# Kernel optimization log

Measured on AMD Instinct MI355X. Metric: run time of the kernel, lower is better.

## Reference

```python
import jax, jax.numpy as jnp
import numpy as np

N_NODES = 50000
N_EDGES = 800000
IN_CH = 128
OUT_CH = 64
H1, C1 = 8, 8            # conv1: heads=8, out=8, concat -> 64
H2, C2 = 1, OUT_CH       # conv2: heads=1, out=64, concat=False
NEG_SLOPE = 0.2


def gat_conv(x, src, dst, W, att_src, att_dst, bias, heads, ch, concat):
    """PyG GATConv (self loops assumed already appended to src/dst).
    x: [N, F_in], W: [F_in, heads*ch], att_*: [heads, ch], bias: [heads*ch] or [ch]."""
    N = x.shape[0]
    h = (x @ W).reshape(N, heads, ch)                       # [N,H,C]
    a_s = jnp.einsum('nhc,hc->nh', h, att_src)              # [N,H]
    a_d = jnp.einsum('nhc,hc->nh', h, att_dst)              # [N,H]
    e = jax.nn.leaky_relu(a_s[src] + a_d[dst], NEG_SLOPE)   # [E,H]
    # segment softmax over incoming edges of each destination node
    m = jax.ops.segment_max(e, dst, num_segments=N)         # [N,H]
    ex = jnp.exp(e - m[dst])
    s = jax.ops.segment_sum(ex, dst, num_segments=N)        # [N,H]
    alpha = ex / (s[dst] + 1e-16)                           # [E,H]
    out = jax.ops.segment_sum(h[src] * alpha[:, :, None], dst, num_segments=N)  # [N,H,C]
    out = out.reshape(N, heads * ch) if concat else out.mean(axis=1)
    return out + bias


def setup_inputs() -> dict:
    key = jax.random.key(0)
    ks = jax.random.split(key, 12)
    glorot = lambda k, shape: jax.random.normal(k, shape, jnp.float32) * np.sqrt(2.0 / (shape[0] + shape[-1]))
    x = jax.random.normal(ks[0], (N_NODES, IN_CH), jnp.float32)
    edge_index = jax.random.randint(ks[1], (2, N_EDGES), 0, N_NODES, jnp.int64 if jax.config.read('jax_enable_x64') else jnp.int32).astype(jnp.int32)
    W1 = glorot(ks[2], (IN_CH, H1 * C1))
    att_src1 = glorot(ks[3], (H1, C1))
    att_dst1 = glorot(ks[4], (H1, C1))
    b1 = jnp.zeros((H1 * C1,), jnp.float32)
    W2 = glorot(ks[5], (H1 * C1, H2 * C2))
    att_src2 = glorot(ks[6], (H2, C2))
    att_dst2 = glorot(ks[7], (H2, C2))
    b2 = jnp.zeros((C2,), jnp.float32)
    return {"x": x, "edge_index": edge_index, "W1": W1, "att_src1": att_src1,
            "att_dst1": att_dst1, "b1": b1, "W2": W2, "att_src2": att_src2,
            "att_dst2": att_dst2, "b2": b2}


def reference(x, edge_index, W1, att_src1, att_dst1, b1, W2, att_src2, att_dst2, b2):
    N = x.shape[0]
    loops = jnp.arange(N, dtype=edge_index.dtype)
    src = jnp.concatenate([edge_index[0], loops])  # add_self_loops=True (PyG default)
    dst = jnp.concatenate([edge_index[1], loops])
    h = gat_conv(x, src, dst, W1, att_src1, att_dst1, b1, H1, C1, concat=True)
    h = jax.nn.elu(h)
    # F.dropout(training=self.training): identity in eval mode
    out = gat_conv(h, src, dst, W2, att_src2, att_dst2, b2, H2, C2, concat=False)
    return out
```

## Files before the change

kernel.cpp:

```cpp
#include <hip/hip_runtime.h>

#define NN 50000
#define NE 800000
#define NEG_SLOPE 0.2f

__device__ __forceinline__ float lrelu(float v) { return v > 0.f ? v : NEG_SLOPE * v; }
__device__ __forceinline__ float bf2f(unsigned short u) { return __uint_as_float((unsigned)u << 16); }
__device__ __forceinline__ unsigned short f2bf(float f) {
    unsigned u = __float_as_uint(f);
    return (unsigned short)((u + 0x7FFFu + ((u >> 16) & 1u)) >> 16);
}

__global__ void hist(const int* __restrict__ ei, int* __restrict__ deg,
                     int* __restrict__ rank) {
    int e = blockIdx.x * blockDim.x + threadIdx.x;
    if (e < NE) rank[e] = atomicAdd(&deg[ei[NE + e]], 1);
}

__global__ __launch_bounds__(256) void scan1(const int* __restrict__ deg,
                                             int* __restrict__ offs, int* __restrict__ bsum) {
    __shared__ int tmp[256];
    int i = blockIdx.x * 256 + threadIdx.x;
    int v = (i < NN) ? deg[i] : 0;
    tmp[threadIdx.x] = v;
    __syncthreads();
    for (int o = 1; o < 256; o <<= 1) {
        int t = (threadIdx.x >= o) ? tmp[threadIdx.x - o] : 0;
        __syncthreads();
        tmp[threadIdx.x] += t;
        __syncthreads();
    }
    if (i < NN) offs[i] = tmp[threadIdx.x] - v;
    if (threadIdx.x == 255) bsum[blockIdx.x] = tmp[255];
}

__global__ __launch_bounds__(256) void scan2(int* __restrict__ bsum) {
    __shared__ int tmp[256];
    int v = bsum[threadIdx.x];
    tmp[threadIdx.x] = v;
    __syncthreads();
    for (int o = 1; o < 256; o <<= 1) {
        int t = (threadIdx.x >= o) ? tmp[threadIdx.x - o] : 0;
        __syncthreads();
        tmp[threadIdx.x] += t;
        __syncthreads();
    }
    bsum[threadIdx.x] = tmp[threadIdx.x] - v;
}

__global__ void scan3(int* __restrict__ offs, const int* __restrict__ bsum) {
    int i = blockIdx.x * blockDim.x + threadIdx.x;
    if (i < NN) offs[i] += bsum[i >> 8];
}

__global__ void scatter(const int* __restrict__ ei, const int* __restrict__ rank,
                        const int* __restrict__ offs, int* __restrict__ srclist) {
    int e = blockIdx.x * blockDim.x + threadIdx.x;
    if (e < NE) {
        int d = ei[NE + e];
        srclist[offs[d] + rank[e]] = ei[e];
    }
}

__global__ void prep(const float* __restrict__ W1, const float* __restrict__ W2,
                     float* __restrict__ W1S, float* __restrict__ W2S) {
    int tid = blockIdx.x * blockDim.x + threadIdx.x;
    if (tid < 8192) {
        int k = tid >> 6, c = tid & 63;
        W1S[((k >> 2) * 64 + c) * 4 + (k & 3)] = W1[k * 64 + c];
    } else if (tid < 12288) {
        int t = tid - 8192;
        int k = t >> 6, c = t & 63;
        W2S[((k >> 2) * 64 + c) * 4 + (k & 3)] = W2[k * 64 + c];
    }
}

__global__ __launch_bounds__(256) void gemm1(const float* __restrict__ x,
                                             const float* __restrict__ W1S,
                                             const float* __restrict__ att_s,
                                             const float* __restrict__ att_d,
                                             unsigned short* __restrict__ h1b,
                                             float* __restrict__ a_s,
                                             float2* __restrict__ nd1) {
    int lane = threadIdx.x & 63;
    int wv   = __builtin_amdgcn_readfirstlane(threadIdx.x >> 6);
    int n0   = blockIdx.x * 16 + wv * 4;
    const float* __restrict__ xr = x + (size_t)n0 * 128;
    const float4* __restrict__ wp = (const float4*)W1S;
    float4 acc = {0.f, 0.f, 0.f, 0.f};
#pragma unroll 4
    for (int k4 = 0; k4 < 32; ++k4) {
        float4 w = wp[k4 * 64 + lane];
        const float* xk = xr + k4 * 4;
        acc.x += xk[0]   * w.x + xk[1]   * w.y + xk[2]   * w.z + xk[3]   * w.w;
        acc.y += xk[128] * w.x + xk[129] * w.y + xk[130] * w.z + xk[131] * w.w;
        acc.z += xk[256] * w.x + xk[257] * w.y + xk[258] * w.z + xk[259] * w.w;
        acc.w += xk[384] * w.x + xk[385] * w.y + xk[386] * w.z + xk[387] * w.w;
    }
    float as_l = att_s[lane], ad_l = att_d[lane];
    float av[4] = {acc.x, acc.y, acc.z, acc.w};
#pragma unroll
    for (int r = 0; r < 4; ++r) {
        float a = av[r];
        h1b[(size_t)(n0 + r) * 64 + lane] = f2bf(a);
        float ps = a * as_l, pd = a * ad_l;
        ps += __shfl_xor(ps, 1, 64); pd += __shfl_xor(pd, 1, 64);
        ps += __shfl_xor(ps, 2, 64); pd += __shfl_xor(pd, 2, 64);
        ps += __shfl_xor(ps, 4, 64); pd += __shfl_xor(pd, 4, 64);
        if ((lane & 7) == 0) {
            int h = lane >> 3;
            a_s[(n0 + r) * 8 + h] = ps;
            nd1[(n0 + r) * 8 + h] = make_float2(pd, lrelu(ps + pd));
        }
    }
}

__global__ __launch_bounds__(256) void agg1(const int* __restrict__ srclist,
                                            const int* __restrict__ offs,
                                            const int* __restrict__ degv,
                                            const float* __restrict__ a_s,
                                            const float2* __restrict__ nd1,
                                            const unsigned short* __restrict__ h1b,
                                            const float* __restrict__ b1,
                                            float* __restrict__ xh) {
    int wv   = threadIdx.x >> 6;
    int lane = threadIdx.x & 63;
    int d    = blockIdx.x * 4 + wv;
    int base = offs[d], dg = degv[d];
    int sub  = lane >> 3, hch = lane & 7;
    float2 nd = nd1[d * 8 + hch];
    float acc0 = 0.f, acc1 = 0.f, acc2 = 0.f, acc3 = 0.f;
    float acc4 = 0.f, acc5 = 0.f, acc6 = 0.f, acc7 = 0.f;
    float sm = 0.f;
#pragma unroll 2
    for (int k = sub; k < dg; k += 8) {
        int s = srclist[base + k];
        float ex = __expf(lrelu(a_s[s * 8 + hch] + nd.x) - nd.y);
        uint4 hv = *(const uint4*)&h1b[(size_t)s * 64 + hch * 8];
        acc0 += __uint_as_float(hv.x << 16)          * ex;
        acc1 += __uint_as_float(hv.x & 0xffff0000u)  * ex;
        acc2 += __uint_as_float(hv.y << 16)          * ex;
        acc3 += __uint_as_float(hv.y & 0xffff0000u)  * ex;
        acc4 += __uint_as_float(hv.z << 16)          * ex;
        acc5 += __uint_as_float(hv.z & 0xffff0000u)  * ex;
        acc6 += __uint_as_float(hv.w << 16)          * ex;
        acc7 += __uint_as_float(hv.w & 0xffff0000u)  * ex;
        sm += ex;
    }
    if (sub == 0) {
        uint4 hv = *(const uint4*)&h1b[(size_t)d * 64 + hch * 8];
        acc0 += __uint_as_float(hv.x << 16);
        acc1 += __uint_as_float(hv.x & 0xffff0000u);
        acc2 += __uint_as_float(hv.y << 16);
        acc3 += __uint_as_float(hv.y & 0xffff0000u);
        acc4 += __uint_as_float(hv.z << 16);
        acc5 += __uint_as_float(hv.z & 0xffff0000u);
        acc6 += __uint_as_float(hv.w << 16);
        acc7 += __uint_as_float(hv.w & 0xffff0000u);
        sm += 1.f;
    }
#pragma unroll
    for (int m = 8; m < 64; m <<= 1) {
        acc0 += __shfl_xor(acc0, m, 64); acc1 += __shfl_xor(acc1, m, 64);
        acc2 += __shfl_xor(acc2, m, 64); acc3 += __shfl_xor(acc3, m, 64);
        acc4 += __shfl_xor(acc4, m, 64); acc5 += __shfl_xor(acc5, m, 64);
        acc6 += __shfl_xor(acc6, m, 64); acc7 += __shfl_xor(acc7, m, 64);
        sm   += __shfl_xor(sm, m, 64);
    }
    if (lane < 8) {
        float inv = 1.f / sm;
        float4 bl = *(const float4*)&b1[lane * 8];
        float4 bh = *(const float4*)&b1[lane * 8 + 4];
        float4 lo, hi;
        lo.x = acc0 * inv + bl.x; lo.x = lo.x > 0.f ? lo.x : expm1f(lo.x);
        lo.y = acc1 * inv + bl.y; lo.y = lo.y > 0.f ? lo.y : expm1f(lo.y);
        lo.z = acc2 * inv + bl.z; lo.z = lo.z > 0.f ? lo.z : expm1f(lo.z);
        lo.w = acc3 * inv + bl.w; lo.w = lo.w > 0.f ? lo.w : expm1f(lo.w);
        hi.x = acc4 * inv + bh.x; hi.x = hi.x > 0.f ? hi.x : expm1f(hi.x);
        hi.y = acc5 * inv + bh.y; hi.y = hi.y > 0.f ? hi.y : expm1f(hi.y);
        hi.z = acc6 * inv + bh.z; hi.z = hi.z > 0.f ? hi.z : expm1f(hi.z);
        hi.w = acc7 * inv + bh.w; hi.w = hi.w > 0.f ? hi.w : expm1f(hi.w);
        *(float4*)&xh[(size_t)d * 64 + lane * 8]     = lo;
        *(float4*)&xh[(size_t)d * 64 + lane * 8 + 4] = hi;
    }
}

__global__ __launch_bounds__(256) void gemm2(const float* __restrict__ xh,
                                             const float* __restrict__ W2S,
                                             const float* __restrict__ att_s,
                                             const float* __restrict__ att_d,
                                             unsigned short* __restrict__ h2b,
                                             float* __restrict__ a_s2,
                                             float2* __restrict__ nd2) {
    int lane = threadIdx.x & 63;
    int wv   = __builtin_amdgcn_readfirstlane(threadIdx.x >> 6);
    int n0   = blockIdx.x * 16 + wv * 4;
    const float* __restrict__ xr = xh + (size_t)n0 * 64;
    const float4* __restrict__ wp = (const float4*)W2S;
    float4 acc = {0.f, 0.f, 0.f, 0.f};
#pragma unroll 4
    for (int k4 = 0; k4 < 16; ++k4) {
        float4 w = wp[k4 * 64 + lane];
        const float* xk = xr + k4 * 4;
        acc.x += xk[0]   * w.x + xk[1]   * w.y + xk[2]   * w.z + xk[3]   * w.w;
        acc.y += xk[64]  * w.x + xk[65]  * w.y + xk[66]  * w.z + xk[67]  * w.w;
        acc.z += xk[128] * w.x + xk[129] * w.y + xk[130] * w.z + xk[131] * w.w;
        acc.w += xk[192] * w.x + xk[193] * w.y + xk[194] * w.z + xk[195] * w.w;
    }
    float as_l = att_s[lane], ad_l = att_d[lane];
    float av[4] = {acc.x, acc.y, acc.z, acc.w};
#pragma unroll
    for (int r = 0; r < 4; ++r) {
        float a = av[r];
        h2b[(size_t)(n0 + r) * 64 + lane] = f2bf(a);
        float ps = a * as_l, pd = a * ad_l;
#pragma unroll
        for (int m = 1; m < 64; m <<= 1) { ps += __shfl_xor(ps, m, 64); pd += __shfl_xor(pd, m, 64); }
        if (lane == 0) {
            a_s2[n0 + r] = ps;
            nd2[n0 + r]  = make_float2(pd, lrelu(ps + pd));
        }
    }
}

__global__ __launch_bounds__(256) void agg2(const int* __restrict__ srclist,
                                            const int* __restrict__ offs,
                                            const int* __restrict__ degv,
                                            const float* __restrict__ a_s2,
                                            const float2* __restrict__ nd2,
                                            const unsigned short* __restrict__ h2b,
                                            const float* __restrict__ b2,
                                            float* __restrict__ out) {
    int wv   = threadIdx.x >> 6;
    int lane = threadIdx.x & 63;
    int d    = blockIdx.x * 4 + wv;
    int base = offs[d], dg = degv[d];
    int sub  = lane >> 3, hch = lane & 7;
    float2 nd = nd2[d];
    float acc0 = 0.f, acc1 = 0.f, acc2 = 0.f, acc3 = 0.f;
    float acc4 = 0.f, acc5 = 0.f, acc6 = 0.f, acc7 = 0.f;
    float sm = 0.f;
#pragma unroll 2
    for (int k = sub; k < dg; k += 8) {
        int s = srclist[base + k];
        float ex = __expf(lrelu(a_s2[s] + nd.x) - nd.y);
        uint4 hv = *(const uint4*)&h2b[(size_t)s * 64 + hch * 8];
        acc0 += __uint_as_float(hv.x << 16)          * ex;
        acc1 += __uint_as_float(hv.x & 0xffff0000u)  * ex;
        acc2 += __uint_as_float(hv.y << 16)          * ex;
        acc3 += __uint_as_float(hv.y & 0xffff0000u)  * ex;
        acc4 += __uint_as_float(hv.z << 16)          * ex;
        acc5 += __uint_as_float(hv.z & 0xffff0000u)  * ex;
        acc6 += __uint_as_float(hv.w << 16)          * ex;
        acc7 += __uint_as_float(hv.w & 0xffff0000u)  * ex;
        sm += ex;
    }
    if (sub == 0) {
        uint4 hv = *(const uint4*)&h2b[(size_t)d * 64 + hch * 8];
        acc0 += __uint_as_float(hv.x << 16);
        acc1 += __uint_as_float(hv.x & 0xffff0000u);
        acc2 += __uint_as_float(hv.y << 16);
        acc3 += __uint_as_float(hv.y & 0xffff0000u);
        acc4 += __uint_as_float(hv.z << 16);
        acc5 += __uint_as_float(hv.z & 0xffff0000u);
        acc6 += __uint_as_float(hv.w << 16);
        acc7 += __uint_as_float(hv.w & 0xffff0000u);
        sm += 1.f;
    }
#pragma unroll
    for (int m = 8; m < 64; m <<= 1) {
        acc0 += __shfl_xor(acc0, m, 64); acc1 += __shfl_xor(acc1, m, 64);
        acc2 += __shfl_xor(acc2, m, 64); acc3 += __shfl_xor(acc3, m, 64);
        acc4 += __shfl_xor(acc4, m, 64); acc5 += __shfl_xor(acc5, m, 64);
        acc6 += __shfl_xor(acc6, m, 64); acc7 += __shfl_xor(acc7, m, 64);
        sm   += __shfl_xor(sm, m, 64);
    }
    if (lane < 8) {
        float inv = 1.f / sm;
        float4 bl = *(const float4*)&b2[lane * 8];
        float4 bh = *(const float4*)&b2[lane * 8 + 4];
        float4 lo, hi;
        lo.x = acc0 * inv + bl.x; lo.y = acc1 * inv + bl.y;
        lo.z = acc2 * inv + bl.z; lo.w = acc3 * inv + bl.w;
        hi.x = acc4 * inv + bh.x; hi.y = acc5 * inv + bh.y;
        hi.z = acc6 * inv + bh.z; hi.w = acc7 * inv + bh.w;
        *(float4*)&out[(size_t)d * 64 + lane * 8]     = lo;
        *(float4*)&out[(size_t)d * 64 + lane * 8 + 4] = hi;
    }
}

extern "C" void kernel_launch(void* const* d_in, const int* in_sizes, int n_in,
                              void* d_out, int out_size, void* d_ws, size_t ws_size,
                              hipStream_t stream) {
    const float* x   = (const float*)d_in[0];
    const int*   ei  = (const int*)d_in[1];
    const float* W1  = (const float*)d_in[2];
    const float* as1 = (const float*)d_in[3];
    const float* ad1 = (const float*)d_in[4];
    const float* b1  = (const float*)d_in[5];
    const float* W2  = (const float*)d_in[6];
    const float* as2 = (const float*)d_in[7];
    const float* ad2 = (const float*)d_in[8];
    const float* b2  = (const float*)d_in[9];
    float* out = (float*)d_out;

    float* ws = (float*)d_ws;
    unsigned short* h1b = (unsigned short*)ws;
    unsigned short* h2b = (unsigned short*)(ws + 1600000);
    float*  xh   = ws + 3200000;
    float*  a_s1 = ws + 6400000;
    float2* nd1  = (float2*)(ws + 6800000);
    float*  a_s2 = ws + 7600000;
    float2* nd2  = (float2*)(ws + 7650000);
    int* deg     = (int*)(ws + 7750000);
    int* offs    = deg + 50000;
    int* bsum    = offs + 50000;
    int* rank    = bsum + 256;
    int* srclist = rank + 800000;
    float* W1S   = (float*)(srclist + 800000);
    float* W2S   = W1S + 8192;

    hipMemsetAsync(deg, 0, (size_t)NN * 4, stream);
    hist<<<3125, 256, 0, stream>>>(ei, deg, rank);
    prep<<<48, 256, 0, stream>>>(W1, W2, W1S, W2S);
    scan1<<<256, 256, 0, stream>>>(deg, offs, bsum);
    scan2<<<1, 256, 0, stream>>>(bsum);
    scan3<<<196, 256, 0, stream>>>(offs, bsum);
    scatter<<<3125, 256, 0, stream>>>(ei, rank, offs, srclist);

    gemm1<<<3125, 256, 0, stream>>>(x, W1S, as1, ad1, h1b, a_s1, nd1);
    agg1<<<12500, 256, 0, stream>>>(srclist, offs, deg, a_s1, nd1, h1b, b1, xh);

    gemm2<<<3125, 256, 0, stream>>>(xh, W2S, as2, ad2, h2b, a_s2, nd2);
    agg2<<<12500, 256, 0, stream>>>(srclist, offs, deg, a_s2, nd2, h2b, b2, out);
}
```

Measured before the change: 168.8 us.

## Reorder second GAT layer to aggregate before projection and fold attention into W2

Removes the gemm2 kernel. The second-layer attention logits come from x·(W2·att), precomputed as vectors and evaluated in agg1. agg2 now aggregates the 64-wide bf16 hidden features and applies W2 once per destination node, using readlane broadcasts. The scan is collapsed into a single kernel using an atomic global cursor, which is valid because CSR segments need not be ordered by node. The memset and prep kernels are merged into one setup kernel. This cuts kernel launches and the xh fp32 write/read traffic, at the cost of extra matmul work inside agg2 and a non-deterministic node-to-segment placement.

```diff
diff --git a/kernel.cpp b/kernel.cpp
--- a/kernel.cpp
+++ b/kernel.cpp
@@ -10,6 +10,42 @@
     unsigned u = __float_as_uint(f);
     return (unsigned short)((u + 0x7FFFu + ((u >> 16) & 1u)) >> 16);
 }
+__device__ __forceinline__ float rlane(float v, int l) {
+    return __int_as_float(__builtin_amdgcn_readlane(__float_as_int(v), l));
+}
+
+__global__ __launch_bounds__(256) void setup(const float* __restrict__ W1,
+                                             const float* __restrict__ W2,
+                                             const float* __restrict__ as2,
+                                             const float* __restrict__ ad2,
+                                             int4* __restrict__ deg4,
+                                             int* __restrict__ gcursor,
+                                             float* __restrict__ W1S,
+                                             float* __restrict__ W2S,
+                                             float* __restrict__ w_as2,
+                                             float* __restrict__ w_ad2) {
+    int gid = blockIdx.x * 256 + threadIdx.x;
+    if (gid < 12500) deg4[gid] = make_int4(0, 0, 0, 0);
+    if (gid == 0) *gcursor = 0;
+    if (gid < 8192) {
+        int k = gid >> 6, c = gid & 63;
+        W1S[((k >> 2) * 64 + c) * 4 + (k & 3)] = W1[k * 64 + c];
+    } else if (gid < 12288) {
+        int t = gid - 8192;
+        int k = t >> 6, c = t & 63;
+        W2S[((k >> 2) * 64 + c) * 4 + (k & 3)] = W2[k * 64 + c];
+    }
+    if (gid < 64) {
+        float s = 0.f;
+        for (int c = 0; c < 64; ++c) s += W2[gid * 64 + c] * as2[c];
+        w_as2[gid] = s;
+    } else if (gid < 128) {
+        int k = gid - 64;
+        float s = 0.f;
+        for (int c = 0; c < 64; ++c) s += W2[k * 64 + c] * ad2[c];
+        w_ad2[k] = s;
+    }
+}
 
 __global__ void hist(const int* __restrict__ ei, int* __restrict__ deg,
                      int* __restrict__ rank) {
@@ -17,9 +53,11 @@
     if (e < NE) rank[e] = atomicAdd(&deg[ei[NE + e]], 1);
 }
 
-__global__ __launch_bounds__(256) void scan1(const int* __restrict__ deg,
-                                             int* __restrict__ offs, int* __restrict__ bsum) {
+__global__ __launch_bounds__(256) void scanA(const int* __restrict__ deg,
+                                             int* __restrict__ offs,
+                                             int* __restrict__ gcursor) {
     __shared__ int tmp[256];
+    __shared__ int base;
     int i = blockIdx.x * 256 + threadIdx.x;
     int v = (i < NN) ? deg[i] : 0;
     tmp[threadIdx.x] = v;
@@ -30,27 +68,9 @@
         tmp[threadIdx.x] += t;
         __syncthreads();
     }
-    if (i < NN) offs[i] = tmp[threadIdx.x] - v;
-    if (threadIdx.x == 255) bsum[blockIdx.x] = tmp[255];
-}
-
-__global__ __launch_bounds__(256) void scan2(int* __restrict__ bsum) {
-    __shared__ int tmp[256];
-    int v = bsum[threadIdx.x];
-    tmp[threadIdx.x] = v;
+    if (threadIdx.x == 255) base = atomicAdd(gcursor, tmp[255]);
     __syncthreads();
-    for (int o = 1; o < 256; o <<= 1) {
-        int t = (threadIdx.x >= o) ? tmp[threadIdx.x - o] : 0;
-        __syncthreads();
-        tmp[threadIdx.x] += t;
-        __syncthreads();
-    }
-    bsum[threadIdx.x] = tmp[threadIdx.x] - v;
-}
-
-__global__ void scan3(int* __restrict__ offs, const int* __restrict__ bsum) {
-    int i = blockIdx.x * blockDim.x + threadIdx.x;
-    if (i < NN) offs[i] += bsum[i >> 8];
+    if (i < NN) offs[i] = base + tmp[threadIdx.x] - v;
 }
 
 __global__ void scatter(const int* __restrict__ ei, const int* __restrict__ rank,
@@ -59,19 +79,6 @@
     if (e < NE) {
         int d = ei[NE + e];
         srclist[offs[d] + rank[e]] = ei[e];
-    }
-}
-
-__global__ void prep(const float* __restrict__ W1, const float* __restrict__ W2,
-                     float* __restrict__ W1S, float* __restrict__ W2S) {
-    int tid = blockIdx.x * blockDim.x + threadIdx.x;
-    if (tid < 8192) {
-        int k = tid >> 6, c = tid & 63;
-        W1S[((k >> 2) * 64 + c) * 4 + (k & 3)] = W1[k * 64 + c];
-    } else if (tid < 12288) {
-        int t = tid - 8192;
-        int k = t >> 6, c = t & 63;
-        W2S[((k >> 2) * 64 + c) * 4 + (k & 3)] = W2[k * 64 + c];
     }
 }
 
@@ -122,7 +129,11 @@
                                             const float2* __restrict__ nd1,
                                             const unsigned short* __restrict__ h1b,
                                             const float* __restrict__ b1,
-                                            float* __restrict__ xh) {
+                                            const float* __restrict__ w_as2,
+                                            const float* __restrict__ w_ad2,
+                                            unsigned short* __restrict__ xhb,
+                                            float* __restrict__ a_s2,
+                                            float2* __restrict__ nd2) {
     int wv   = threadIdx.x >> 6;
     int lane = threadIdx.x & 63;
     int d    = blockIdx.x * 4 + wv;
@@ -167,59 +178,39 @@
         acc6 += __shfl_xor(acc6, m, 64); acc7 += __shfl_xor(acc7, m, 64);
         sm   += __shfl_xor(sm, m, 64);
     }
+    float inv = 1.f / sm;
+    int li = (lane & 7) * 8;
+    float4 bl = *(const float4*)&b1[li];
+    float4 bh = *(const float4*)&b1[li + 4];
+    float4 lo, hi;
+    lo.x = acc0 * inv + bl.x; lo.x = lo.x > 0.f ? lo.x : expm1f(lo.x);
+    lo.y = acc1 * inv + bl.y; lo.y = lo.y > 0.f ? lo.y : expm1f(lo.y);
+    lo.z = acc2 * inv + bl.z; lo.z = lo.z > 0.f ? lo.z : expm1f(lo.z);
+    lo.w = acc3 * inv + bl.w; lo.w = lo.w > 0.f ? lo.w : expm1f(lo.w);
+    hi.x = acc4 * inv + bh.x; hi.x = hi.x > 0.f ? hi.x : expm1f(hi.x);
+    hi.y = acc5 * inv + bh.y; hi.y = hi.y > 0.f ? hi.y : expm1f(hi.y);
+    hi.z = acc6 * inv + bh.z; hi.z = hi.z > 0.f ? hi.z : expm1f(hi.z);
+    hi.w = acc7 * inv + bh.w; hi.w = hi.w > 0.f ? hi.w : expm1f(hi.w);
     if (lane < 8) {
-        float inv = 1.f / sm;
-        float4 bl = *(const float4*)&b1[lane * 8];
-        float4 bh = *(const float4*)&b1[lane * 8 + 4];
-        float4 lo, hi;
-        lo.x = acc0 * inv + bl.x; lo.x = lo.x > 0.f ? lo.x : expm1f(lo.x);
-        lo.y = acc1 * inv + bl.y; lo.y = lo.y > 0.f ? lo.y : expm1f(lo.y);
-        lo.z = acc2 * inv + bl.z; lo.z = lo.z > 0.f ? lo.z : expm1f(lo.z);
-        lo.w = acc3 * inv + bl.w; lo.w = lo.w > 0.f ? lo.w : expm1f(lo.w);
-        hi.x = acc4 * inv + bh.x; hi.x = hi.x > 0.f ? hi.x : expm1f(hi.x);
-        hi.y = acc5 * inv + bh.y; hi.y = hi.y > 0.f ? hi.y : expm1f(hi.y);
-        hi.z = acc6 * inv + bh.z; hi.z = hi.z > 0.f ? hi.z : expm1f(hi.z);
-        hi.w = acc7 * inv + bh.w; hi.w = hi.w > 0.f ? hi.w : expm1f(hi.w);
-        *(float4*)&xh[(size_t)d * 64 + lane * 8]     = lo;
-        *(float4*)&xh[(size_t)d * 64 + lane * 8 + 4] = hi;
-    }
-}
-
-__global__ __launch_bounds__(256) void gemm2(const float* __restrict__ xh,
-                                             const float* __restrict__ W2S,
-                                             const float* __restrict__ att_s,
-                                             const float* __restrict__ att_d,
-                                             unsigned short* __restrict__ h2b,
-                                             float* __restrict__ a_s2,
-                                             float2* __restrict__ nd2) {
-    int lane = threadIdx.x & 63;
-    int wv   = __builtin_amdgcn_readfirstlane(threadIdx.x >> 6);
-    int n0   = blockIdx.x * 16 + wv * 4;
-    const float* __restrict__ xr = xh + (size_t)n0 * 64;
-    const float4* __restrict__ wp = (const float4*)W2S;
-    float4 acc = {0.f, 0.f, 0.f, 0.f};
-#pragma unroll 4
-    for (int k4 = 0; k4 < 16; ++k4) {
-        float4 w = wp[k4 * 64 + lane];
-        const float* xk = xr + k4 * 4;
-        acc.x += xk[0]   * w.x + xk[1]   * w.y + xk[2]   * w.z + xk[3]   * w.w;
-        acc.y += xk[64]  * w.x + xk[65]  * w.y + xk[66]  * w.z + xk[67]  * w.w;
-        acc.z += xk[128] * w.x + xk[129] * w.y + xk[130] * w.z + xk[131] * w.w;
-        acc.w += xk[192] * w.x + xk[193] * w.y + xk[194] * w.z + xk[195] * w.w;
-    }
-    float as_l = att_s[lane], ad_l = att_d[lane];
-    float av[4] = {acc.x, acc.y, acc.z, acc.w};
-#pragma unroll
-    for (int r = 0; r < 4; ++r) {
-        float a = av[r];
-        h2b[(size_t)(n0 + r) * 64 + lane] = f2bf(a);
-        float ps = a * as_l, pd = a * ad_l;
-#pragma unroll
-        for (int m = 1; m < 64; m <<= 1) { ps += __shfl_xor(ps, m, 64); pd += __shfl_xor(pd, m, 64); }
-        if (lane == 0) {
-            a_s2[n0 + r] = ps;
-            nd2[n0 + r]  = make_float2(pd, lrelu(ps + pd));
-        }
+        uint4 pk;
+        pk.x = ((unsigned)f2bf(lo.y) << 16) | f2bf(lo.x);
+        pk.y = ((unsigned)f2bf(lo.w) << 16) | f2bf(lo.z);
+        pk.z = ((unsigned)f2bf(hi.y) << 16) | f2bf(hi.x);
+        pk.w = ((unsigned)f2bf(hi.w) << 16) | f2bf(hi.z);
+        *(uint4*)&xhb[(size_t)d * 64 + lane * 8] = pk;
+    }
+    float4 s0 = *(const float4*)&w_as2[li], s1 = *(const float4*)&w_as2[li + 4];
+    float4 d0 = *(const float4*)&w_ad2[li], d1 = *(const float4*)&w_ad2[li + 4];
+    float ps = lo.x*s0.x + lo.y*s0.y + lo.z*s0.z + lo.w*s0.w
+             + hi.x*s1.x + hi.y*s1.y + hi.z*s1.z + hi.w*s1.w;
+    float pd = lo.x*d0.x + lo.y*d0.y + lo.z*d0.z + lo.w*d0.w
+             + hi.x*d1.x + hi.y*d1.y + hi.z*d1.z + hi.w*d1.w;
+    ps += __shfl_xor(ps, 1, 64); pd += __shfl_xor(pd, 1, 64);
+    ps += __shfl_xor(ps, 2, 64); pd += __shfl_xor(pd, 2, 64);
+    ps += __shfl_xor(ps, 4, 64); pd += __shfl_xor(pd, 4, 64);
+    if (lane == 0) {
+        a_s2[d] = ps;
+        nd2[d]  = make_float2(pd, lrelu(ps + pd));
     }
 }
 
@@ -228,7 +219,8 @@
                                             const int* __restrict__ degv,
                                             const float* __restrict__ a_s2,
                                             const float2* __restrict__ nd2,
-                                            const unsigned short* __restrict__ h2b,
+                                            const unsigned short* __restrict__ xhb,
+                                            const float* __restrict__ W2S,
                                             const float* __restrict__ b2,
                                             float* __restrict__ out) {
     int wv   = threadIdx.x >> 6;
@@ -244,7 +236,7 @@
     for (int k = sub; k < dg; k += 8) {
         int s = srclist[base + k];
         float ex = __expf(lrelu(a_s2[s] + nd.x) - nd.y);
-        uint4 hv = *(const uint4*)&h2b[(size_t)s * 64 + hch * 8];
+        uint4 hv = *(const uint4*)&xhb[(size_t)s * 64 + hch * 8];
         acc0 += __uint_as_float(hv.x << 16)          * ex;
         acc1 += __uint_as_float(hv.x & 0xffff0000u)  * ex;
         acc2 += __uint_as_float(hv.y << 16)          * ex;
@@ -256,7 +248,7 @@
         sm += ex;
     }
     if (sub == 0) {
-        uint4 hv = *(const uint4*)&h2b[(size_t)d * 64 + hch * 8];
+        uint4 hv = *(const uint4*)&xhb[(size_t)d * 64 + hch * 8];
         acc0 += __uint_as_float(hv.x << 16);
         acc1 += __uint_as_float(hv.x & 0xffff0000u);
         acc2 += __uint_as_float(hv.y << 16);
@@ -275,18 +267,21 @@
         acc6 += __shfl_xor(acc6, m, 64); acc7 += __shfl_xor(acc7, m, 64);
         sm   += __shfl_xor(sm, m, 64);
     }
-    if (lane < 8) {
-        float inv = 1.f / sm;
-        float4 bl = *(const float4*)&b2[lane * 8];
-        float4 bh = *(const float4*)&b2[lane * 8 + 4];
-        float4 lo, hi;
-        lo.x = acc0 * inv + bl.x; lo.y = acc1 * inv + bl.y;
-        lo.z = acc2 * inv + bl.z; lo.w = acc3 * inv + bl.w;
-        hi.x = acc4 * inv + bh.x; hi.y = acc5 * inv + bh.y;
-        hi.z = acc6 * inv + bh.z; hi.w = acc7 * inv + bh.w;
-        *(float4*)&out[(size_t)d * 64 + lane * 8]     = lo;
-        *(float4*)&out[(size_t)d * 64 + lane * 8 + 4] = hi;
-    }
+    float inv = 1.f / sm;
+    float t0 = acc0 * inv, t1 = acc1 * inv, t2 = acc2 * inv, t3 = acc3 * inv;
+    float t4 = acc4 * inv, t5 = acc5 * inv, t6 = acc6 * inv, t7 = acc7 * inv;
+    const float4* wp = (const float4*)W2S;
+    float o = 0.f;
+#pragma unroll
+    for (int k4 = 0; k4 < 16; ++k4) {
+        float4 w = wp[k4 * 64 + lane];
+        int j = k4 >> 1;
+        if (k4 & 1)
+            o += rlane(t4, j) * w.x + rlane(t5, j) * w.y + rlane(t6, j) * w.z + rlane(t7, j) * w.w;
+        else
+            o += rlane(t0, j) * w.x + rlane(t1, j) * w.y + rlane(t2, j) * w.z + rlane(t3, j) * w.w;
+    }
+    out[(size_t)d * 64 + lane] = o + b2[lane];
 }
 
 extern "C" void kernel_launch(void* const* d_in, const int* in_sizes, int n_in,
@@ -306,31 +301,30 @@
 
     float* ws = (float*)d_ws;
     unsigned short* h1b = (unsigned short*)ws;
-    unsigned short* h2b = (unsigned short*)(ws + 1600000);
-    float*  xh   = ws + 3200000;
-    float*  a_s1 = ws + 6400000;
-    float2* nd1  = (float2*)(ws + 6800000);
-    float*  a_s2 = ws + 7600000;
-    float2* nd2  = (float2*)(ws + 7650000);
-    int* deg     = (int*)(ws + 7750000);
+    unsigned short* xhb = (unsigned short*)(ws + 1600000);
+    float*  a_s1 = ws + 3200000;
+    float2* nd1  = (float2*)(ws + 3600000);
+    float*  a_s2 = ws + 4400000;
+    float2* nd2  = (float2*)(ws + 4450000);
+    int* deg     = (int*)(ws + 4550000);
     int* offs    = deg + 50000;
-    int* bsum    = offs + 50000;
-    int* rank    = bsum + 256;
+    int* gcursor = offs + 50000;
+    int* rank    = gcursor + 64;
     int* srclist = rank + 800000;
     float* W1S   = (float*)(srclist + 800000);
     float* W2S   = W1S + 8192;
-
-    hipMemsetAsync(deg, 0, (size_t)NN * 4, stream);
+    float* w_as2 = W2S + 4096;
+    float* w_ad2 = w_as2 + 64;
+
+    setup<<<49, 256, 0, stream>>>(W1, W2, as2, ad2, (int4*)deg, gcursor,
+                                  W1S, W2S, w_as2, w_ad2);
     hist<<<3125, 256, 0, stream>>>(ei, deg, rank);
-    prep<<<48, 256, 0, stream>>>(W1, W2, W1S, W2S);
-    scan1<<<256, 256, 0, stream>>>(deg, offs, bsum);
-    scan2<<<1, 256, 0, stream>>>(bsum);
-    scan3<<<196, 256, 0, stream>>>(offs, bsum);
+    scanA<<<196, 256, 0, stream>>>(deg, offs, gcursor);
     scatter<<<3125, 256, 0, stream>>>(ei, rank, offs, srclist);
 
     gemm1<<<3125, 256, 0, stream>>>(x, W1S, as1, ad1, h1b, a_s1, nd1);
-    agg1<<<12500, 256, 0, stream>>>(srclist, offs, deg, a_s1, nd1, h1b, b1, xh);
-
-    gemm2<<<3125, 256, 0, stream>>>(xh, W2S, as2, ad2, h2b, a_s2, nd2);
-    agg2<<<12500, 256, 0, stream>>>(srclist, offs, deg, a_s2, nd2, h2b, b2, out);
-}
+    agg1<<<12500, 256, 0, stream>>>(srclist, offs, deg, a_s1, nd1, h1b, b1,
+                                    w_as2, w_ad2, xhb, a_s2, nd2);
+
+    agg2<<<12500, 256, 0, stream>>>(srclist, offs, deg, a_s2, nd2, xhb, W2S, b2, out);
+}
```

Result: no change. 169.8 us (+0.5%).
